# Performance work log

Measured on AMD Instinct MI355X. Metric: run time of the kernel, lower is better.

Reference implementation:

```python
import jax, jax.numpy as jnp
import numpy as np

BITS = 8
QMAX = float(2 ** (BITS - 1) - 1)   # 127
QMIN = -float(2 ** (BITS - 1))      # -128
LORA_SCALING = 2.0                  # alpha=16 / r=8


def fake_quant(x):
    """Per-tensor symmetric fake quantization with STE (STE irrelevant for fwd)."""
    scale = jnp.maximum(jnp.max(jnp.abs(x)) / QMAX, 1e-8)
    y = jnp.clip(jnp.round(x / scale), QMIN, QMAX) * scale
    return x + jax.lax.stop_gradient(y - x)


def qat_linear_lora(x, W, b, A, B):
    # fake-quantized main path + full-precision LoRA path
    xq = fake_quant(x)
    Wq = fake_quant(W)
    main = jnp.einsum('bsi,oi->bso', xq, Wq) + b
    lora = jnp.einsum('bsr,or->bso', jnp.einsum('bsi,ri->bsr', x, A), B) * LORA_SCALING
    return main + lora


def setup_inputs() -> dict:
    key = jax.random.key(0)
    ks = jax.random.split(key, 6)
    n_embd, d_ff, r = 1024, 4096, 8
    B_, S = 4, 2048
    return {
        'hidden_states': jax.random.normal(ks[0], (B_, S, n_embd), jnp.float32),
        'W_fc': jax.random.normal(ks[1], (d_ff, n_embd), jnp.float32) * 0.02,
        'b_fc': jnp.zeros((d_ff,), jnp.float32),
        'A_fc': jax.random.normal(ks[2], (r, n_embd), jnp.float32) * (1.0 / n_embd) ** 0.5,
        'B_fc': jnp.zeros((d_ff, r), jnp.float32),
        'W_proj': jax.random.normal(ks[3], (n_embd, d_ff), jnp.float32) * 0.02,
        'b_proj': jnp.zeros((n_embd,), jnp.float32),
        'A_proj': jax.random.normal(ks[4], (r, d_ff), jnp.float32) * (1.0 / d_ff) ** 0.5,
        'B_proj': jnp.zeros((n_embd, r), jnp.float32),
    }


def reference(hidden_states, W_fc, b_fc, A_fc, B_fc, W_proj, b_proj, A_proj, B_proj):
    h = qat_linear_lora(hidden_states, W_fc, b_fc, A_fc, B_fc)
    h = jax.nn.gelu(h, approximate=False)  # nn.GELU() default = exact erf GELU
    h = qat_linear_lora(h, W_proj, b_proj, A_proj, B_proj)
    return h
```

## Files before the change

kernel.cpp:

```cpp
#include <hip/hip_runtime.h>
#include <hip/hip_bf16.h>
#include <hip/hip_fp16.h>
#include <math.h>


typedef unsigned short u16;
typedef unsigned int u32;
typedef signed char i8;
typedef int i32x4 __attribute__((ext_vector_type(4)));
typedef _Float16 f16;
typedef f16 f16x8 __attribute__((ext_vector_type(8)));
typedef float f32x4 __attribute__((ext_vector_type(4)));

#define ASYNC16(gp, lp)                                                        \
  __builtin_amdgcn_global_load_lds(                                            \
      (__attribute__((address_space(1))) void*)(gp),                           \
      (__attribute__((address_space(3))) void*)(lp), 16, 0, 0)

#define VMCNT(N) asm volatile("s_waitcnt vmcnt(" #N ")" ::: "memory")
#define LGKM0 asm volatile("s_waitcnt lgkmcnt(0)" ::: "memory")
#define SBAR __builtin_amdgcn_s_barrier()

__device__ __forceinline__ int quanti(float v, float inv) {
  float q = rintf(v * inv);
  q = fminf(fmaxf(q, -128.0f), 127.0f);
  return (int)q;
}

__device__ __forceinline__ u32 pack4(float4 v, float inv) {
  return ((u32)(quanti(v.x, inv) & 255)) |
         ((u32)(quanti(v.y, inv) & 255) << 8) |
         ((u32)(quanti(v.z, inv) & 255) << 16) |
         ((u32)(quanti(v.w, inv) & 255) << 24);
}

__device__ __forceinline__ float load_scale(const u32* slot) {
  return fmaxf(__uint_as_float(*slot) * (1.0f / 127.0f), 1e-8f);
}

__device__ __forceinline__ float gelu_erf(float v) {
  float z = fabsf(v) * 0.70710678118654752f;
  float t = __builtin_amdgcn_rcpf(fmaf(0.3275911f, z, 1.0f));
  float poly =
      t * fmaf(t,
               fmaf(t,
                    fmaf(t, fmaf(t, 1.061405429f, -1.453152027f),
                         1.421413741f),
                    -0.284496736f),
               0.254829592f);
  float e = fmaf(-poly, exp2f(-z * z * 1.4426950408889634f), 1.0f);
  return 0.5f * v * fmaf(copysignf(e, v), 1.0f, 1.0f);
}

__global__ void absmax_kernel(const float* __restrict__ x, int n4,
                              u32* __restrict__ slot) {
  float m = 0.0f;
  int stride = gridDim.x * blockDim.x;
  for (int i = blockIdx.x * blockDim.x + threadIdx.x; i < n4; i += stride) {
    float4 v = ((const float4*)x)[i];
    m = fmaxf(m, fmaxf(fmaxf(fabsf(v.x), fabsf(v.y)),
                       fmaxf(fabsf(v.z), fabsf(v.w))));
  }
#pragma unroll
  for (int off = 32; off > 0; off >>= 1) m = fmaxf(m, __shfl_down(m, off));
  __shared__ float wmax[4];
  int lane = threadIdx.x & 63, wave = threadIdx.x >> 6;
  if (lane == 0) wmax[wave] = m;
  __syncthreads();
  if (threadIdx.x == 0) {
    m = fmaxf(fmaxf(wmax[0], wmax[1]), fmaxf(wmax[2], wmax[3]));
    atomicMax(slot, __float_as_uint(m));
  }
}

__global__ void quant_w_kernel(const float* __restrict__ w, int n16,
                               const u32* __restrict__ slot,
                               i8* __restrict__ q) {
  float inv = 1.0f / load_scale(slot);
  int stride = gridDim.x * blockDim.x;
  for (int i = blockIdx.x * blockDim.x + threadIdx.x; i < n16; i += stride) {
    const float4* src = (const float4*)w + i * 4;
    u32 pk[4];
#pragma unroll
    for (int c = 0; c < 4; c++) pk[c] = pack4(src[c], inv);
    uint4 o = {pk[0], pk[1], pk[2], pk[3]};
    ((uint4*)q)[i] = o;
  }
}

__global__ void conv_a16_kernel(const float* __restrict__ A,
                                f16* __restrict__ Ah, int ncols) {
  int i = blockIdx.x * blockDim.x + threadIdx.x;
  int base = i * 8;
  if (base >= 16 * ncols) return;
  if (base < 8 * ncols) {
    float4 v0 = ((const float4*)(A + base))[0];
    float4 v1 = ((const float4*)(A + base))[1];
    f16x8 o = {(f16)v0.x, (f16)v0.y, (f16)v0.z, (f16)v0.w,
               (f16)v1.x, (f16)v1.y, (f16)v1.z, (f16)v1.w};
    *(f16x8*)(Ah + base) = o;
  } else {
    f16x8 z = {};
    *(f16x8*)(Ah + base) = z;
  }
}

__launch_bounds__(256) __global__
    void quant_x_t1_fused(const float* __restrict__ x,
                          const f16* __restrict__ Ah,
                          const u32* __restrict__ slot,
                          i8* __restrict__ xq,
                          float* __restrict__ t1) {
  int tid = threadIdx.x;
  int lane = tid & 63, wave = tid >> 6;
  int quad = lane >> 4, l15 = lane & 15;
  int bx = blockIdx.x;
  long m0 = (long)blockIdx.y * 64 + wave * 16;
  long row = m0 + l15;
  int k0 = bx * 512;
  float inv = 1.0f / load_scale(slot);

  const float* xp = x + row * 1024 + k0 + quad * 8;
  const f16* ap = Ah + l15 * 1024 + k0 + quad * 8;
  i8* op = xq + row * 1024 + k0 + quad * 8;
  f32x4 acc = {0.0f, 0.0f, 0.0f, 0.0f};
#pragma unroll
  for (int s = 0; s < 16; s++) {
    float4 v0 = ((const float4*)(xp + s * 32))[0];
    float4 v1 = ((const float4*)(xp + s * 32))[1];
    f16x8 af = {(f16)v0.x, (f16)v0.y, (f16)v0.z, (f16)v0.w,
                (f16)v1.x, (f16)v1.y, (f16)v1.z, (f16)v1.w};
    f16x8 bf = *(const f16x8*)(ap + s * 32);
    acc = __builtin_amdgcn_mfma_f32_16x16x32_f16(af, bf, acc, 0, 0, 0);
    uint2 o = {pack4(v0, inv), pack4(v1, inv)};
    *(uint2*)(op + s * 32) = o;
  }
  if (l15 < 8) {
#pragma unroll
    for (int r = 0; r < 4; r++) {
      long m = m0 + quad * 4 + r;
      atomicAdd(&t1[m * 8 + l15], acc[r]);
    }
  }
}

__launch_bounds__(256) __global__
    void quant_h_t2_fused(u16* __restrict__ h,
                          const f16* __restrict__ Ah,
                          const u32* __restrict__ slot,
                          float* __restrict__ t2) {
  int tid = threadIdx.x;
  int lane = tid & 63, wave = tid >> 6;
  int quad = lane >> 4, l15 = lane & 15;
  int bx = blockIdx.x;
  long m0 = (long)blockIdx.y * 64 + wave * 16;
  long row = m0 + l15;
  int k0 = bx * 512;
  float inv = 1.0f / load_scale(slot);

  const u16* hp = h + row * 4096 + k0 + quad * 8;
  const f16* ap = Ah + l15 * 4096 + k0 + quad * 8;
  f32x4 acc = {0.0f, 0.0f, 0.0f, 0.0f};
  u32 q[32];
#pragma unroll
  for (int s = 0; s < 16; s++) {
    uint4 hv = *(const uint4*)(hp + s * 32);
    f16x8 af = *(const f16x8*)&hv;
    f16x8 bf = *(const f16x8*)(ap + s * 32);
    acc = __builtin_amdgcn_mfma_f32_16x16x32_f16(af, bf, acc, 0, 0, 0);
    u32 uu[4] = {hv.x, hv.y, hv.z, hv.w};
#pragma unroll
    for (int c = 0; c < 2; c++) {
      float2 f0 = __half22float2(*(__half2*)&uu[2 * c]);
      float2 f1 = __half22float2(*(__half2*)&uu[2 * c + 1]);
      q[2 * s + c] = ((u32)(quanti(f0.x, inv) & 255)) |
                     ((u32)(quanti(f0.y, inv) & 255) << 8) |
                     ((u32)(quanti(f1.x, inv) & 255) << 16) |
                     ((u32)(quanti(f1.y, inv) & 255) << 24);
    }
  }
  asm volatile("" ::: "memory");
  i8* op = (i8*)h + row * 8192 + bx * 1024 + quad * 8;
#pragma unroll
  for (int s = 0; s < 16; s++) {
    uint2 o = {q[2 * s], q[2 * s + 1]};
    *(uint2*)(op + s * 32) = o;
  }
  if (l15 < 8) {
#pragma unroll
    for (int r = 0; r < 4; r++) {
      long m = m0 + quad * 4 + r;
      atomicAdd(&t2[m * 8 + l15], acc[r]);
    }
  }
}

template <int MODE, int BN, int WARPS_M>
__launch_bounds__(512, 2) __global__
    void gemm8p_kernel(const i8* __restrict__ A, const i8* __restrict__ B,
                       int N, int K, int lda, int ldb,
                       const float* __restrict__ bias,
                       const float* __restrict__ tl,
                       const float* __restrict__ Bl,
                       const u32* __restrict__ scales, int sa, int sb,
                       void* __restrict__ outp, u32* __restrict__ hmax) {
  constexpr int WARPS_N = 8 / WARPS_M;
  constexpr int MT = 256 / (16 * WARPS_M);
  constexpr int NT = BN / (16 * WARPS_N);
  constexpr int LB = BN / 128;
  __shared__ __align__(16) i8 As[2][256 * 128];
  __shared__ __align__(16) i8 Bs[2][BN * 128];
  __shared__ u32 bmax;
  int tid = threadIdx.x;
  int lane = tid & 63, wave = tid >> 6;
  int quad = lane >> 4, l15 = lane & 15;
  int wm = (wave % WARPS_M) * (MT * 16);
  int wn = (wave / WARPS_M) * (NT * 16);
  int nwg = gridDim.x * gridDim.y;
  int lin = blockIdx.y * gridDim.x + blockIdx.x;
  int swb = (lin & 7) * (nwg >> 3) + (lin >> 3);
  int bx = swb % gridDim.x, by = swb / gridDim.x;
  long m0 = (long)by * 256;
  long n0 = (long)bx * BN;
  if (MODE == 0 && tid == 0) bmax = 0u;

  const i8* pA[2];
  int ldsA[2];
#pragma unroll
  for (int u = 0; u < 2; u++) {
    int c = u * 512 + tid;
    int row = c >> 3;
    int swz = ((c & 7) ^ (row & 7)) * 16;
    pA[u] = A + (m0 + row) * lda + swz;
    ldsA[u] = c * 16;
  }
  const i8* pB[LB];
  int ldsB[LB];
#pragma unroll
  for (int u = 0; u < LB; u++) {
    int c = u * 512 + tid;
    int row = c >> 3;
    int swz = ((c & 7) ^ (row & 7)) * 16;
    pB[u] = B + (n0 + row) * ldb + swz;
    ldsB[u] = c * 16;
  }

  auto stageA = [&](int t, int h) {
    int kb = (MODE == 1) ? ((t >> 2) * 1024 + (t & 3) * 128) : (t << 7);
    int bb = t & 1;
#pragma unroll
    for (int u = 0; u < 2; u++)
      ASYNC16(pA[u] + (long)h * 128 * lda + kb,
              &As[bb][h * 16384 + ldsA[u]]);
  };
  auto stageB = [&](int t, int h) {
    int kb = t << 7;
    int bb = t & 1;
#pragma unroll
    for (int u = 0; u < LB; u++)
      ASYNC16(pB[u] + (long)h * (BN / 2) * ldb + kb,
              &Bs[bb][h * (BN / 2) * 128 + ldsB[u]]);
  };

  int s0 = (quad ^ (l15 & 7)) * 16;
  int s1 = s0 ^ 64;

  i32x4 acc[MT][NT] = {};
  int NTILES = K >> 7;

  stageA(0, 0); stageA(0, 1); stageB(0, 0); stageB(0, 1);
  stageA(1, 0); stageA(1, 1);
  VMCNT(4);
  SBAR;

  for (int t = 0; t < NTILES; t++) {
    const i8* Ab = As[t & 1];
    const i8* Bb = Bs[t & 1];
    i32x4 a0[MT], a1[MT], b0[NT], b1[NT];
#pragma unroll
    for (int i = 0; i < MT; i++)
      a0[i] = *(const i32x4*)(Ab + (wm + i * 16 + l15) * 128 + s0);
#pragma unroll
    for (int j = 0; j < NT; j++)
      b0[j] = *(const i32x4*)(Bb + (wn + j * 16 + l15) * 128 + s0);
    if (t + 1 < NTILES) stageB(t + 1, 0);
    SBAR;
    LGKM0;
    __builtin_amdgcn_s_setprio(1);
#pragma unroll
    for (int i = 0; i < MT / 2; i++)
#pragma unroll
      for (int j = 0; j < NT; j++)
        acc[i][j] = __builtin_amdgcn_mfma_i32_16x16x64_i8(a0[i], b0[j],
                                                          acc[i][j], 0, 0, 0);
    __builtin_amdgcn_s_setprio(0);
    SBAR;
#pragma unroll
    for (int i = 0; i < MT; i++)
      a1[i] = *(const i32x4*)(Ab + (wm + i * 16 + l15) * 128 + s1);
    if (t + 1 < NTILES) stageB(t + 1, 1);
    SBAR;
    LGKM0;
    __builtin_amdgcn_s_setprio(1);
#pragma unroll
    for (int i = MT / 2; i < MT; i++)
#pragma unroll
      for (int j = 0; j < NT; j++)
        acc[i][j] = __builtin_amdgcn_mfma_i32_16x16x64_i8(a0[i], b0[j],
                                                          acc[i][j], 0, 0, 0);
    __builtin_amdgcn_s_setprio(0);
    SBAR;
#pragma unroll
    for (int j = 0; j < NT; j++)
      b1[j] = *(const i32x4*)(Bb + (wn + j * 16 + l15) * 128 + s1);
    if (t + 2 < NTILES) stageA(t + 2, 0);
    SBAR;
    LGKM0;
    __builtin_amdgcn_s_setprio(1);
#pragma unroll
    for (int i = 0; i < MT / 2; i++)
#pragma unroll
      for (int j = 0; j < NT; j++)
        acc[i][j] = __builtin_amdgcn_mfma_i32_16x16x64_i8(a1[i], b1[j],
                                                          acc[i][j], 0, 0, 0);
    __builtin_amdgcn_s_setprio(0);
    SBAR;
    if (t + 2 < NTILES) stageA(t + 2, 1);
    SBAR;
    __builtin_amdgcn_s_setprio(1);
#pragma unroll
    for (int i = MT / 2; i < MT; i++)
#pragma unroll
      for (int j = 0; j < NT; j++)
        acc[i][j] = __builtin_amdgcn_mfma_i32_16x16x64_i8(a1[i], b1[j],
                                                          acc[i][j], 0, 0, 0);
    __builtin_amdgcn_s_setprio(0);
    if (t + 2 < NTILES) {
      VMCNT(4);
    } else {
      VMCNT(0);
    }
    SBAR;
  }

  float scale = load_scale(scales + sa) * load_scale(scales + sb);
  float biasv[NT];
  float4 bl0[NT], bl1[NT];
#pragma unroll
  for (int j = 0; j < NT; j++) {
    long n = n0 + wn + j * 16 + l15;
    biasv[j] = bias[n];
    bl0[j] = ((const float4*)(Bl + n * 8))[0];
    bl1[j] = ((const float4*)(Bl + n * 8))[1];
  }
  float lmax = 0.0f;
#pragma unroll
  for (int i = 0; i < MT; i++) {
#pragma unroll
    for (int r = 0; r < 4; r++) {
      long m = m0 + wm + i * 16 + quad * 4 + r;
      float4 t0 = ((const float4*)(tl + m * 8))[0];
      float4 t1v = ((const float4*)(tl + m * 8))[1];
#pragma unroll
      for (int j = 0; j < NT; j++) {
        long n = n0 + wn + j * 16 + l15;
        float lora = t0.x * bl0[j].x + t0.y * bl0[j].y + t0.z * bl0[j].z +
                     t0.w * bl0[j].w + t1v.x * bl1[j].x + t1v.y * bl1[j].y +
                     t1v.z * bl1[j].z + t1v.w * bl1[j].w;
        float v = (float)acc[i][j][r] * scale + biasv[j] + 2.0f * lora;
        if (MODE == 0) {
          float hv = gelu_erf(v);
          __half hh = __float2half_rn(hv);
          ((u16*)outp)[m * N + n] = *(u16*)&hh;
          lmax = fmaxf(lmax, fabsf(hv));
        } else {
          ((float*)outp)[m * N + n] = v;
        }
      }
    }
  }
  if (MODE == 0) {
    atomicMax(&bmax, __float_as_uint(lmax));
    __syncthreads();
    if (tid == 0) atomicMax(hmax, bmax);
  }
}

extern "C" void kernel_launch(void* const* d_in, const int* in_sizes, int n_in,
                              void* d_out, int out_size, void* d_ws,
                              size_t ws_size, hipStream_t stream) {
  const float* x = (const float*)d_in[0];
  const float* Wfc = (const float*)d_in[1];
  const float* bfc = (const float*)d_in[2];
  const float* Afc = (const float*)d_in[3];
  const float* Bfc = (const float*)d_in[4];
  const float* Wpr = (const float*)d_in[5];
  const float* bpr = (const float*)d_in[6];
  const float* Apr = (const float*)d_in[7];
  const float* Bpr = (const float*)d_in[8];
  float* out = (float*)d_out;

  char* w = (char*)d_ws;
  u32* scales = (u32*)w;
  float* t1 = (float*)(w + 256);
  float* t2 = (float*)(w + 256 + 262144);
  i8* xq = (i8*)(w + 524544);
  f16* aprh = (f16*)(w + 8913152);
  f16* afch = (f16*)(w + 9175040);
  i8* wq1 = (i8*)(w + 9437184);
  i8* wq2 = (i8*)(w + 13631488);
  u16* hq = (u16*)(w + 17825792);
  if (ws_size < 84934656) return;

  hipMemsetAsync(w, 0, 524544, stream);
  conv_a16_kernel<<<32, 256, 0, stream>>>(Apr, aprh, 4096);
  conv_a16_kernel<<<8, 256, 0, stream>>>(Afc, afch, 1024);
  absmax_kernel<<<1024, 256, 0, stream>>>(x, 8192 * 1024 / 4, scales + 0);
  absmax_kernel<<<512, 256, 0, stream>>>(Wfc, 4096 * 1024 / 4, scales + 1);
  absmax_kernel<<<512, 256, 0, stream>>>(Wpr, 4096 * 1024 / 4, scales + 2);
  quant_x_t1_fused<<<dim3(2, 128), 256, 0, stream>>>(x, afch, scales + 0, xq,
                                                     t1);
  quant_w_kernel<<<256, 256, 0, stream>>>(Wfc, 4096 * 1024 / 16, scales + 1,
                                          wq1);
  quant_w_kernel<<<256, 256, 0, stream>>>(Wpr, 4096 * 1024 / 16, scales + 2,
                                          wq2);
  gemm8p_kernel<0, 256, 2><<<dim3(16, 32), 512, 0, stream>>>(
      xq, wq1, 4096, 1024, 1024, 1024, bfc, t1, Bfc, scales, 0, 1, hq,
      scales + 3);
  quant_h_t2_fused<<<dim3(8, 128), 256, 0, stream>>>(hq, aprh, scales + 3, t2);
  gemm8p_kernel<1, 128, 4><<<dim3(8, 32), 512, 0, stream>>>(
      (const i8*)hq, wq2, 1024, 4096, 8192, 4096, bpr, t2, Bpr, scales, 3, 2,
      out, nullptr);
}
```

Baseline: 306.8 us.

## Replace 8-wave 256-row GEMM with 4-wave 128x128 tile kernel

Both int8 GEMMs move from a 512-thread kernel with 256-row tiles and an 8-phase ping-pong schedule to a 256-thread kernel with 128x128 tiles, 4x4 MFMA tiles per wave and a simpler 2-phase schedule. The grids grow to match, which raises workgroup count and likely occupancy, since LDS per block drops to 64KB. The cost is lower data reuse per tile, which means more global and LDS traffic per MFMA. The tile and scheduling change also risks the epilogue indexing, which is not shown here, no longer matching the new layout.

Result: no change. 304.7 us (-0.7%).

```diff
diff --git a/kernel.cpp b/kernel.cpp
--- a/kernel.cpp
+++ b/kernel.cpp
@@ -195,71 +195,57 @@
   }
 }
 
-template <int MODE, int BN, int WARPS_M>
-__launch_bounds__(512, 2) __global__
-    void gemm8p_kernel(const i8* __restrict__ A, const i8* __restrict__ B,
+template <int MODE>
+__launch_bounds__(256, 2) __global__
+    void gemm4w_kernel(const i8* __restrict__ A, const i8* __restrict__ B,
                        int N, int K, int lda, int ldb,
                        const float* __restrict__ bias,
                        const float* __restrict__ tl,
                        const float* __restrict__ Bl,
                        const u32* __restrict__ scales, int sa, int sb,
                        void* __restrict__ outp, u32* __restrict__ hmax) {
-  constexpr int WARPS_N = 8 / WARPS_M;
-  constexpr int MT = 256 / (16 * WARPS_M);
-  constexpr int NT = BN / (16 * WARPS_N);
-  constexpr int LB = BN / 128;
-  __shared__ __align__(16) i8 As[2][256 * 128];
-  __shared__ __align__(16) i8 Bs[2][BN * 128];
+  constexpr int MT = 4, NT = 4;
+  __shared__ __align__(16) i8 As[2][128 * 128];
+  __shared__ __align__(16) i8 Bs[2][128 * 128];
   __shared__ u32 bmax;
   int tid = threadIdx.x;
   int lane = tid & 63, wave = tid >> 6;
   int quad = lane >> 4, l15 = lane & 15;
-  int wm = (wave % WARPS_M) * (MT * 16);
-  int wn = (wave / WARPS_M) * (NT * 16);
+  int wm = (wave & 1) * 64, wn = (wave >> 1) * 64;
   int nwg = gridDim.x * gridDim.y;
   int lin = blockIdx.y * gridDim.x + blockIdx.x;
   int swb = (lin & 7) * (nwg >> 3) + (lin >> 3);
   int bx = swb % gridDim.x, by = swb / gridDim.x;
-  long m0 = (long)by * 256;
-  long n0 = (long)bx * BN;
+  long m0 = (long)by * 128;
+  long n0 = (long)bx * 128;
   if (MODE == 0 && tid == 0) bmax = 0u;
 
   const i8* pA[2];
-  int ldsA[2];
+  const i8* pB[2];
+  int ldsOff[2];
 #pragma unroll
   for (int u = 0; u < 2; u++) {
-    int c = u * 512 + tid;
+    int c = u * 256 + tid;
     int row = c >> 3;
     int swz = ((c & 7) ^ (row & 7)) * 16;
     pA[u] = A + (m0 + row) * lda + swz;
-    ldsA[u] = c * 16;
-  }
-  const i8* pB[LB];
-  int ldsB[LB];
-#pragma unroll
-  for (int u = 0; u < LB; u++) {
-    int c = u * 512 + tid;
-    int row = c >> 3;
-    int swz = ((c & 7) ^ (row & 7)) * 16;
     pB[u] = B + (n0 + row) * ldb + swz;
-    ldsB[u] = c * 16;
+    ldsOff[u] = c * 16;
   }
 
   auto stageA = [&](int t, int h) {
     int kb = (MODE == 1) ? ((t >> 2) * 1024 + (t & 3) * 128) : (t << 7);
-    int bb = t & 1;
 #pragma unroll
     for (int u = 0; u < 2; u++)
-      ASYNC16(pA[u] + (long)h * 128 * lda + kb,
-              &As[bb][h * 16384 + ldsA[u]]);
+      ASYNC16(pA[u] + (long)h * 64 * lda + kb,
+              &As[t & 1][h * 8192 + ldsOff[u]]);
   };
   auto stageB = [&](int t, int h) {
     int kb = t << 7;
-    int bb = t & 1;
-#pragma unroll
-    for (int u = 0; u < LB; u++)
-      ASYNC16(pB[u] + (long)h * (BN / 2) * ldb + kb,
-              &Bs[bb][h * (BN / 2) * 128 + ldsB[u]]);
+#pragma unroll
+    for (int u = 0; u < 2; u++)
+      ASYNC16(pB[u] + (long)h * 64 * ldb + kb,
+              &Bs[t & 1][h * 8192 + ldsOff[u]]);
   };
 
   int s0 = (quad ^ (l15 & 7)) * 16;
@@ -278,17 +264,19 @@
     const i8* Bb = Bs[t & 1];
     i32x4 a0[MT], a1[MT], b0[NT], b1[NT];
 #pragma unroll
-    for (int i = 0; i < MT; i++)
+    for (int i = 0; i < MT; i++) {
       a0[i] = *(const i32x4*)(Ab + (wm + i * 16 + l15) * 128 + s0);
+      a1[i] = *(const i32x4*)(Ab + (wm + i * 16 + l15) * 128 + s1);
+    }
 #pragma unroll
     for (int j = 0; j < NT; j++)
       b0[j] = *(const i32x4*)(Bb + (wn + j * 16 + l15) * 128 + s0);
-    if (t + 1 < NTILES) stageB(t + 1, 0);
+    if (t + 1 < NTILES) { stageB(t + 1, 0); stageB(t + 1, 1); }
     SBAR;
     LGKM0;
     __builtin_amdgcn_s_setprio(1);
 #pragma unroll
-    for (int i = 0; i < MT / 2; i++)
+    for (int i = 0; i < MT; i++)
 #pragma unroll
       for (int j = 0; j < NT; j++)
         acc[i][j] = __builtin_amdgcn_mfma_i32_16x16x64_i8(a0[i], b0[j],
@@ -296,40 +284,14 @@
     __builtin_amdgcn_s_setprio(0);
     SBAR;
 #pragma unroll
-    for (int i = 0; i < MT; i++)
-      a1[i] = *(const i32x4*)(Ab + (wm + i * 16 + l15) * 128 + s1);
-    if (t + 1 < NTILES) stageB(t + 1, 1);
+    for (int j = 0; j < NT; j++)
+      b1[j] = *(const i32x4*)(Bb + (wn + j * 16 + l15) * 128 + s1);
+    if (t + 2 < NTILES) { stageA(t + 2, 0); stageA(t + 2, 1); }
     SBAR;
     LGKM0;
     __builtin_amdgcn_s_setprio(1);
 #pragma unroll
-    for (int i = MT / 2; i < MT; i++)
-#pragma unroll
-      for (int j = 0; j < NT; j++)
-        acc[i][j] = __builtin_amdgcn_mfma_i32_16x16x64_i8(a0[i], b0[j],
-                                                          acc[i][j], 0, 0, 0);
-    __builtin_amdgcn_s_setprio(0);
-    SBAR;
-#pragma unroll
-    for (int j = 0; j < NT; j++)
-      b1[j] = *(const i32x4*)(Bb + (wn + j * 16 + l15) * 128 + s1);
-    if (t + 2 < NTILES) stageA(t + 2, 0);
-    SBAR;
-    LGKM0;
-    __builtin_amdgcn_s_setprio(1);
-#pragma unroll
-    for (int i = 0; i < MT / 2; i++)
-#pragma unroll
-      for (int j = 0; j < NT; j++)
-        acc[i][j] = __builtin_amdgcn_mfma_i32_16x16x64_i8(a1[i], b1[j],
-                                                          acc[i][j], 0, 0, 0);
-    __builtin_amdgcn_s_setprio(0);
-    SBAR;
-    if (t + 2 < NTILES) stageA(t + 2, 1);
-    SBAR;
-    __builtin_amdgcn_s_setprio(1);
-#pragma unroll
-    for (int i = MT / 2; i < MT; i++)
+    for (int i = 0; i < MT; i++)
 #pragma unroll
       for (int j = 0; j < NT; j++)
         acc[i][j] = __builtin_amdgcn_mfma_i32_16x16x64_i8(a1[i], b1[j],
@@ -424,11 +386,11 @@
                                           wq1);
   quant_w_kernel<<<256, 256, 0, stream>>>(Wpr, 4096 * 1024 / 16, scales + 2,
                                           wq2);
-  gemm8p_kernel<0, 256, 2><<<dim3(16, 32), 512, 0, stream>>>(
+  gemm4w_kernel<0><<<dim3(32, 64), 256, 0, stream>>>(
       xq, wq1, 4096, 1024, 1024, 1024, bfc, t1, Bfc, scales, 0, 1, hq,
       scales + 3);
   quant_h_t2_fused<<<dim3(8, 128), 256, 0, stream>>>(hq, aprh, scales + 3, t2);
-  gemm8p_kernel<1, 128, 4><<<dim3(8, 32), 512, 0, stream>>>(
+  gemm4w_kernel<1><<<dim3(8, 64), 256, 0, stream>>>(
       (const i8*)hq, wq2, 1024, 4096, 8192, 4096, bpr, t2, Bpr, scales, 3, 2,
       out, nullptr);
 }
```

## Batch small prep kernels, swap MFMA operands for vectorized GEMM epilogue stores

Applied to the files above, without the earlier changes.

Merges the two A-conversion launches, three absmax launches and two weight-quant launches into single multi-tensor launches indexed by blockIdx.y, cutting launch overhead and filling the GPU better. Swaps the MFMA operand order so each lane's accumulator holds four consecutive output columns. The epilogue can then write packed half4 or float4 stores instead of scalar ones, with bias and LoRA-B loaded per column group. It also adds a sched_barrier after the LDS wait to pin instruction scheduling. The absmax grid for x is halved (512 blocks instead of 1024), which may reduce that pass's parallelism.

After: 411.9 us. +34.2%, slower.

```diff
diff --git a/kernel.cpp b/kernel.cpp
--- a/kernel.cpp
+++ b/kernel.cpp
@@ -18,7 +18,11 @@
       (__attribute__((address_space(3))) void*)(lp), 16, 0, 0)
 
 #define VMCNT(N) asm volatile("s_waitcnt vmcnt(" #N ")" ::: "memory")
-#define LGKM0 asm volatile("s_waitcnt lgkmcnt(0)" ::: "memory")
+#define LGKM0                                                                  \
+  do {                                                                         \
+    asm volatile("s_waitcnt lgkmcnt(0)" ::: "memory");                         \
+    __builtin_amdgcn_sched_barrier(0);                                         \
+  } while (0)
 #define SBAR __builtin_amdgcn_s_barrier()
 
 __device__ __forceinline__ int quanti(float v, float inv) {
@@ -52,8 +56,16 @@
   return 0.5f * v * fmaf(copysignf(e, v), 1.0f, 1.0f);
 }
 
-__global__ void absmax_kernel(const float* __restrict__ x, int n4,
-                              u32* __restrict__ slot) {
+__global__ void absmax3_kernel(const float* __restrict__ t0, int n0,
+                               const float* __restrict__ t1, int n1,
+                               const float* __restrict__ t2, int n2,
+                               u32* __restrict__ slots) {
+  const float* x;
+  int n4;
+  u32* slot;
+  if (blockIdx.y == 0) { x = t0; n4 = n0; slot = slots + 0; }
+  else if (blockIdx.y == 1) { x = t1; n4 = n1; slot = slots + 1; }
+  else { x = t2; n4 = n2; slot = slots + 2; }
   float m = 0.0f;
   int stride = gridDim.x * blockDim.x;
   for (int i = blockIdx.x * blockDim.x + threadIdx.x; i < n4; i += stride) {
@@ -73,10 +85,13 @@
   }
 }
 
-__global__ void quant_w_kernel(const float* __restrict__ w, int n16,
-                               const u32* __restrict__ slot,
-                               i8* __restrict__ q) {
-  float inv = 1.0f / load_scale(slot);
+__global__ void quant_w2_kernel(const float* __restrict__ w0,
+                                const float* __restrict__ w1, int n16,
+                                const u32* __restrict__ slots,
+                                i8* __restrict__ q0, i8* __restrict__ q1) {
+  const float* w = blockIdx.y ? w1 : w0;
+  i8* q = blockIdx.y ? q1 : q0;
+  float inv = 1.0f / load_scale(slots + 1 + blockIdx.y);
   int stride = gridDim.x * blockDim.x;
   for (int i = blockIdx.x * blockDim.x + threadIdx.x; i < n16; i += stride) {
     const float4* src = (const float4*)w + i * 4;
@@ -88,8 +103,13 @@
   }
 }
 
-__global__ void conv_a16_kernel(const float* __restrict__ A,
-                                f16* __restrict__ Ah, int ncols) {
+__global__ void conv_a16x2_kernel(const float* __restrict__ A0,
+                                  f16* __restrict__ Ah0,
+                                  const float* __restrict__ A1,
+                                  f16* __restrict__ Ah1) {
+  const float* A = blockIdx.y ? A1 : A0;
+  f16* Ah = blockIdx.y ? Ah1 : Ah0;
+  int ncols = blockIdx.y ? 1024 : 4096;
   int i = blockIdx.x * blockDim.x + threadIdx.x;
   int base = i * 8;
   if (base >= 16 * ncols) return;
@@ -291,7 +311,7 @@
     for (int i = 0; i < MT / 2; i++)
 #pragma unroll
       for (int j = 0; j < NT; j++)
-        acc[i][j] = __builtin_amdgcn_mfma_i32_16x16x64_i8(a0[i], b0[j],
+        acc[i][j] = __builtin_amdgcn_mfma_i32_16x16x64_i8(b0[j], a0[i],
                                                           acc[i][j], 0, 0, 0);
     __builtin_amdgcn_s_setprio(0);
     SBAR;
@@ -306,7 +326,7 @@
     for (int i = MT / 2; i < MT; i++)
 #pragma unroll
       for (int j = 0; j < NT; j++)
-        acc[i][j] = __builtin_amdgcn_mfma_i32_16x16x64_i8(a0[i], b0[j],
+        acc[i][j] = __builtin_amdgcn_mfma_i32_16x16x64_i8(b0[j], a0[i],
                                                           acc[i][j], 0, 0, 0);
     __builtin_amdgcn_s_setprio(0);
     SBAR;
@@ -321,7 +341,7 @@
     for (int i = 0; i < MT / 2; i++)
 #pragma unroll
       for (int j = 0; j < NT; j++)
-        acc[i][j] = __builtin_amdgcn_mfma_i32_16x16x64_i8(a1[i], b1[j],
+        acc[i][j] = __builtin_amdgcn_mfma_i32_16x16x64_i8(b1[j], a1[i],
                                                           acc[i][j], 0, 0, 0);
     __builtin_amdgcn_s_setprio(0);
     SBAR;
@@ -332,7 +352,7 @@
     for (int i = MT / 2; i < MT; i++)
 #pragma unroll
       for (int j = 0; j < NT; j++)
-        acc[i][j] = __builtin_amdgcn_mfma_i32_16x16x64_i8(a1[i], b1[j],
+        acc[i][j] = __builtin_amdgcn_mfma_i32_16x16x64_i8(b1[j], a1[i],
                                                           acc[i][j], 0, 0, 0);
     __builtin_amdgcn_s_setprio(0);
     if (t + 2 < NTILES) {
@@ -344,38 +364,47 @@
   }
 
   float scale = load_scale(scales + sa) * load_scale(scales + sb);
-  float biasv[NT];
-  float4 bl0[NT], bl1[NT];
+  float lmax = 0.0f;
 #pragma unroll
   for (int j = 0; j < NT; j++) {
-    long n = n0 + wn + j * 16 + l15;
-    biasv[j] = bias[n];
-    bl0[j] = ((const float4*)(Bl + n * 8))[0];
-    bl1[j] = ((const float4*)(Bl + n * 8))[1];
-  }
-  float lmax = 0.0f;
-#pragma unroll
-  for (int i = 0; i < MT; i++) {
+    long nb = n0 + wn + j * 16 + quad * 4;
+    float4 bv = *(const float4*)(bias + nb);
+    float4 blr[4][2];
 #pragma unroll
     for (int r = 0; r < 4; r++) {
-      long m = m0 + wm + i * 16 + quad * 4 + r;
+      blr[r][0] = ((const float4*)(Bl + (nb + r) * 8))[0];
+      blr[r][1] = ((const float4*)(Bl + (nb + r) * 8))[1];
+    }
+#pragma unroll
+    for (int i = 0; i < MT; i++) {
+      long m = m0 + wm + i * 16 + l15;
       float4 t0 = ((const float4*)(tl + m * 8))[0];
       float4 t1v = ((const float4*)(tl + m * 8))[1];
-#pragma unroll
-      for (int j = 0; j < NT; j++) {
-        long n = n0 + wn + j * 16 + l15;
-        float lora = t0.x * bl0[j].x + t0.y * bl0[j].y + t0.z * bl0[j].z +
-                     t0.w * bl0[j].w + t1v.x * bl1[j].x + t1v.y * bl1[j].y +
-                     t1v.z * bl1[j].z + t1v.w * bl1[j].w;
-        float v = (float)acc[i][j][r] * scale + biasv[j] + 2.0f * lora;
-        if (MODE == 0) {
-          float hv = gelu_erf(v);
-          __half hh = __float2half_rn(hv);
-          ((u16*)outp)[m * N + n] = *(u16*)&hh;
-          lmax = fmaxf(lmax, fabsf(hv));
-        } else {
-          ((float*)outp)[m * N + n] = v;
+      float vout[4];
+#pragma unroll
+      for (int r = 0; r < 4; r++) {
+        float lora = t0.x * blr[r][0].x + t0.y * blr[r][0].y +
+                     t0.z * blr[r][0].z + t0.w * blr[r][0].w +
+                     t1v.x * blr[r][1].x + t1v.y * blr[r][1].y +
+                     t1v.z * blr[r][1].z + t1v.w * blr[r][1].w;
+        float bvr = (r == 0) ? bv.x : (r == 1) ? bv.y : (r == 2) ? bv.z : bv.w;
+        vout[r] = (float)acc[i][j][r] * scale + bvr + 2.0f * lora;
+      }
+      if (MODE == 0) {
+        u32 pk[2];
+#pragma unroll
+        for (int c = 0; c < 2; c++) {
+          float h0 = gelu_erf(vout[2 * c]);
+          float h1 = gelu_erf(vout[2 * c + 1]);
+          lmax = fmaxf(lmax, fmaxf(fabsf(h0), fabsf(h1)));
+          __half a = __float2half_rn(h0), b = __float2half_rn(h1);
+          pk[c] = (u32)(*(u16*)&a) | ((u32)(*(u16*)&b) << 16);
         }
+        uint2 o = {pk[0], pk[1]};
+        *(uint2*)((u16*)outp + m * N + nb) = o;
+      } else {
+        float4 o = {vout[0], vout[1], vout[2], vout[3]};
+        *(float4*)((float*)outp + m * N + nb) = o;
       }
     }
   }
@@ -413,17 +442,13 @@
   if (ws_size < 84934656) return;
 
   hipMemsetAsync(w, 0, 524544, stream);
-  conv_a16_kernel<<<32, 256, 0, stream>>>(Apr, aprh, 4096);
-  conv_a16_kernel<<<8, 256, 0, stream>>>(Afc, afch, 1024);
-  absmax_kernel<<<1024, 256, 0, stream>>>(x, 8192 * 1024 / 4, scales + 0);
-  absmax_kernel<<<512, 256, 0, stream>>>(Wfc, 4096 * 1024 / 4, scales + 1);
-  absmax_kernel<<<512, 256, 0, stream>>>(Wpr, 4096 * 1024 / 4, scales + 2);
+  conv_a16x2_kernel<<<dim3(32, 2), 256, 0, stream>>>(Apr, aprh, Afc, afch);
+  absmax3_kernel<<<dim3(512, 3), 256, 0, stream>>>(
+      x, 8192 * 1024 / 4, Wfc, 4096 * 1024 / 4, Wpr, 4096 * 1024 / 4, scales);
   quant_x_t1_fused<<<dim3(2, 128), 256, 0, stream>>>(x, afch, scales + 0, xq,
                                                      t1);
-  quant_w_kernel<<<256, 256, 0, stream>>>(Wfc, 4096 * 1024 / 16, scales + 1,
-                                          wq1);
-  quant_w_kernel<<<256, 256, 0, stream>>>(Wpr, 4096 * 1024 / 16, scales + 2,
-                                          wq2);
+  quant_w2_kernel<<<dim3(256, 2), 256, 0, stream>>>(Wfc, Wpr, 4096 * 1024 / 16,
+                                                    scales, wq1, wq2);
   gemm8p_kernel<0, 256, 2><<<dim3(16, 32), 512, 0, stream>>>(
       xq, wq1, 4096, 1024, 1024, 1024, bfc, t1, Bfc, scales, 0, 1, hq,
       scales + 3);
```
